# Optimization experiments

Measured on AMD Instinct MI355X. Metric: run time of the kernel, lower is better.

## Reference

```python
import jax, jax.numpy as jnp
import numpy as np
import math
from jax import lax

N, C, D = 16384, 1000, 512
CHUNK = 128  # tile size over samples for the L1 path (avoids NxCxD materialization)
EPS = 1e-8   # torch F.cosine_similarity eps


def setup_inputs() -> dict:
    key = jax.random.key(0)
    kf, kc = jax.random.split(key)
    features = jax.random.normal(kf, (N, D), dtype=jnp.float32)
    centroids = jax.random.normal(kc, (C, D), dtype=jnp.float32)
    return {"features": features, "centroids": centroids}


def _distances(features, centroids):
    n, d = features.shape
    scale = 1.0 / math.sqrt(d)

    # --- L1: cdist(p=1), computed in sample tiles to avoid an [N,C,D] tensor ---
    def l1_chunk(fc):  # fc: [CHUNK, D] -> [CHUNK, C]
        return jnp.sum(jnp.abs(fc[:, None, :] - centroids[None, :, :]), axis=-1)

    f_tiles = features.reshape(-1, CHUNK, d)
    l1 = lax.map(l1_chunk, f_tiles).reshape(n, -1) * scale

    # --- L2: cdist(p=2) via ||f||^2 + ||c||^2 - 2 f.c (GEMM fast path) ---
    f_sq = jnp.sum(features * features, axis=1)            # [N]
    c_sq = jnp.sum(centroids * centroids, axis=1)          # [C]
    dots = features @ centroids.T                          # [N, C]
    sq = jnp.maximum(f_sq[:, None] + c_sq[None, :] - 2.0 * dots, 0.0)
    l2 = jnp.sqrt(sq) * scale

    # --- cosine: F.cosine_similarity with per-vector norm clamped at EPS ---
    f_norm = jnp.maximum(jnp.sqrt(f_sq), EPS)              # [N]
    c_norm = jnp.maximum(jnp.sqrt(c_sq), EPS)              # [C]
    cos = (dots / (f_norm[:, None] * c_norm[None, :])) * scale

    return l1, l2, cos


def reference(features, centroids):
    return _distances(features, centroids)
```

## Files before the change

### kernel.cpp

```cpp
#include <hip/hip_runtime.h>
#include <math.h>

typedef float f32x4 __attribute__((ext_vector_type(4)));
typedef short s16x8 __attribute__((ext_vector_type(8)));

#define N_TOT 16384
#define C_TOT 1000
#define C_PAD 1024
#define D_TOT 512
#define NC ((size_t)N_TOT * C_TOT)

#define EPS_F 1e-8f
#define SCALE_F 0.04419417382415922f

#define GL_LDS(gp, lp)                                                        \
    __builtin_amdgcn_global_load_lds(                                         \
        (const __attribute__((address_space(1))) void*)(gp),                  \
        (__attribute__((address_space(3))) void*)(lp), 16, 0, 0)

__global__ __launch_bounds__(256)
void sq_kernel(const float* __restrict__ F, const float* __restrict__ Cc,
               float* __restrict__ sqout) {
    int gw   = (blockIdx.x * 256 + threadIdx.x) >> 6;
    int lane = threadIdx.x & 63;
    if (gw >= N_TOT + C_TOT) return;
    const float* src = (gw < N_TOT) ? (F + (size_t)gw * D_TOT)
                                    : (Cc + (size_t)(gw - N_TOT) * D_TOT);
    f32x4 a = *(const f32x4*)(src + lane * 4);
    f32x4 b = *(const f32x4*)(src + 256 + lane * 4);
    float acc = a[0] * a[0];
    acc = fmaf(a[1], a[1], acc);
    acc = fmaf(a[2], a[2], acc);
    acc = fmaf(a[3], a[3], acc);
    acc = fmaf(b[0], b[0], acc);
    acc = fmaf(b[1], b[1], acc);
    acc = fmaf(b[2], b[2], acc);
    acc = fmaf(b[3], b[3], acc);
    #pragma unroll
    for (int off = 32; off > 0; off >>= 1)
        acc += __shfl_xor(acc, off);
    if (lane == 0) sqout[gw] = acc;
}

__device__ inline short f2bf(float x) {
    union { float f; unsigned u; } v; v.f = x;
    unsigned r = (v.u + 0x7FFFu + ((v.u >> 16) & 1u)) >> 16;
    return (short)r;
}

__global__ __launch_bounds__(256)
void cvt_kernel(const float* __restrict__ F, const float* __restrict__ Cc,
                short* __restrict__ Fbf, short* __restrict__ Cbf) {
    const int FS8 = N_TOT * D_TOT / 8;
    const int CS8 = C_PAD * D_TOT / 8;
    int gid = blockIdx.x * 256 + threadIdx.x;
    if (gid < FS8) {
        const float* s = F + (size_t)gid * 8;
        f32x4 a = *(const f32x4*)s;
        f32x4 b = *(const f32x4*)(s + 4);
        s16x8 o;
        o[0] = f2bf(a[0]); o[1] = f2bf(a[1]); o[2] = f2bf(a[2]); o[3] = f2bf(a[3]);
        o[4] = f2bf(b[0]); o[5] = f2bf(b[1]); o[6] = f2bf(b[2]); o[7] = f2bf(b[3]);
        *(s16x8*)(Fbf + (size_t)gid * 8) = o;
    } else if (gid < FS8 + CS8) {
        int j = gid - FS8;
        int base = j * 8;
        int crow = base >> 9;
        s16x8 o = (s16x8)(short)0;
        if (crow < C_TOT) {
            const float* s = Cc + (size_t)base;
            f32x4 a = *(const f32x4*)s;
            f32x4 b = *(const f32x4*)(s + 4);
            o[0] = f2bf(a[0]); o[1] = f2bf(a[1]); o[2] = f2bf(a[2]); o[3] = f2bf(a[3]);
            o[4] = f2bf(b[0]); o[5] = f2bf(b[1]); o[6] = f2bf(b[2]); o[7] = f2bf(b[3]);
        }
        *(s16x8*)(Cbf + (size_t)base) = o;
    }
}

__global__ __launch_bounds__(256)
void dot_gemm(const short* __restrict__ Fbf, const short* __restrict__ Cbf,
              const float* __restrict__ sqbuf, float* __restrict__ out) {
    __shared__ short lds[2][8192];

    const int tid  = threadIdx.x;
    const int lane = tid & 63;
    const int wid  = tid >> 6;
    const int wr   = wid >> 1;
    const int wc   = wid & 1;
    const int m0   = blockIdx.y * 128;
    const int n0   = blockIdx.x * 128;

    const int row0 = tid >> 2;
    const int row1 = row0 + 64;
    const int slot = tid & 3;
    const int sw0  = slot ^ ((row0 >> 1) & 3);
    const int sw1  = slot ^ ((row1 >> 1) & 3);
    const short* sA0 = Fbf + (size_t)(m0 + row0) * D_TOT + sw0 * 8;
    const short* sA1 = Fbf + (size_t)(m0 + row1) * D_TOT + sw1 * 8;
    const short* sB0 = Cbf + (size_t)(n0 + row0) * D_TOT + sw0 * 8;
    const short* sB1 = Cbf + (size_t)(n0 + row1) * D_TOT + sw1 * 8;

    int offA[4], offB[4];
    #pragma unroll
    for (int fi = 0; fi < 4; ++fi) {
        int R = wr * 64 + fi * 16 + (lane & 15);
        offA[fi] = R * 32 + (((lane >> 4) ^ ((R >> 1) & 3)) << 3);
    }
    #pragma unroll
    for (int fj = 0; fj < 4; ++fj) {
        int R = wc * 64 + fj * 16 + (lane & 15);
        offB[fj] = 4096 + R * 32 + (((lane >> 4) ^ ((R >> 1) & 3)) << 3);
    }

    f32x4 acc[4][4];
    #pragma unroll
    for (int fi = 0; fi < 4; ++fi)
        #pragma unroll
        for (int fj = 0; fj < 4; ++fj) acc[fi][fj] = (f32x4)(0.f);

    GL_LDS(sA0, &lds[0][(size_t)tid * 8]);
    GL_LDS(sA1, &lds[0][(size_t)(tid + 256) * 8]);
    GL_LDS(sB0, &lds[0][4096 + (size_t)tid * 8]);
    GL_LDS(sB1, &lds[0][4096 + (size_t)(tid + 256) * 8]);
    __syncthreads();

    const int NK = D_TOT / 32;
    for (int kt = 0; kt < NK; ++kt) {
        if (kt + 1 < NK) {
            const int nb = (kt + 1) & 1;
            const int d1 = (kt + 1) * 32;
            GL_LDS(sA0 + d1, &lds[nb][(size_t)tid * 8]);
            GL_LDS(sA1 + d1, &lds[nb][(size_t)(tid + 256) * 8]);
            GL_LDS(sB0 + d1, &lds[nb][4096 + (size_t)tid * 8]);
            GL_LDS(sB1 + d1, &lds[nb][4096 + (size_t)(tid + 256) * 8]);
        }
        const short* lb = lds[kt & 1];
        s16x8 af[4], bg[4];
        #pragma unroll
        for (int fi = 0; fi < 4; ++fi) af[fi] = *(const s16x8*)&lb[offA[fi]];
        #pragma unroll
        for (int fj = 0; fj < 4; ++fj) bg[fj] = *(const s16x8*)&lb[offB[fj]];
        #pragma unroll
        for (int fi = 0; fi < 4; ++fi)
            #pragma unroll
            for (int fj = 0; fj < 4; ++fj)
                acc[fi][fj] = __builtin_amdgcn_mfma_f32_16x16x32_bf16(
                    af[fi], bg[fj], acc[fi][fj], 0, 0, 0);
        __syncthreads();
    }

    const float* csq = sqbuf + N_TOT;
    float fs_[4][4], fn_[4][4];
    #pragma unroll
    for (int fi = 0; fi < 4; ++fi)
        #pragma unroll
        for (int reg = 0; reg < 4; ++reg) {
            int m = m0 + wr * 64 + fi * 16 + ((lane >> 4) << 2) + reg;
            float v = sqbuf[m];
            fs_[fi][reg] = v;
            fn_[fi][reg] = fmaxf(sqrtf(v), EPS_F);
        }
    #pragma unroll
    for (int fj = 0; fj < 4; ++fj) {
        int c = n0 + wc * 64 + fj * 16 + (lane & 15);
        if (c < C_TOT) {
            float cs = csq[c];
            float cn = fmaxf(sqrtf(cs), EPS_F);
            #pragma unroll
            for (int fi = 0; fi < 4; ++fi) {
                int mrow = m0 + wr * 64 + fi * 16 + ((lane >> 4) << 2);
                #pragma unroll
                for (int reg = 0; reg < 4; ++reg) {
                    float d = acc[fi][fj][reg];
                    size_t p = (size_t)(mrow + reg) * C_TOT + c;
                    float sqv = fmaxf(fs_[fi][reg] + cs - 2.0f * d, 0.f);
                    out[NC + p]     = sqrtf(sqv) * SCALE_F;
                    out[2 * NC + p] = (d * SCALE_F) / (fn_[fi][reg] * cn);
                }
            }
        }
    }
}

__device__ inline void add_abs(float& acc, float d) {
    asm("v_add_f32 %0, %0, abs(%1)" : "+v"(acc) : "v"(d));
}

__global__ __launch_bounds__(256)
void l1_main(const float* __restrict__ F, const float* __restrict__ Cc,
             float* __restrict__ out) {
    __shared__ float lds[2][192 * 16];

    const int tid = threadIdx.x;
    const int tx  = tid & 15;
    const int ty  = tid >> 4;
    const int c0  = blockIdx.x * 64;
    const int n0  = blockIdx.y * 128;

    const int srow  = tid >> 2;
    const int sslot = tid & 3;
    const int w16   = (tid >> 6) * 16;

    const float* fA = F + (size_t)(n0 + srow) * D_TOT + sslot * 4;
    const float* fB = fA + (size_t)64 * D_TOT;
    const int cswz  = sslot ^ ((srow >> 2) & 3);
    const float* cP = Cc + (size_t)(c0 + srow) * D_TOT + cswz * 4;
    const bool cok  = (c0 + srow) < C_TOT;

    f32x4 l1v[8];
    #pragma unroll
    for (int i = 0; i < 8; ++i) l1v[i] = (f32x4)(0.f);

    GL_LDS(fA, &lds[0][w16 * 16]);
    GL_LDS(fB, &lds[0][(64 + w16) * 16]);
    if (cok) GL_LDS(cP, &lds[0][(128 + w16) * 16]);
    __syncthreads();

    const int NT  = 32;
    const int crs = (tx >> 2) & 3;

    for (int t = 0; t < NT; ++t) {
        if (t + 1 < NT) {
            const int nb = (t + 1) & 1;
            const int d1 = (t + 1) * 16;
            GL_LDS(fA + d1, &lds[nb][w16 * 16]);
            GL_LDS(fB + d1, &lds[nb][(64 + w16) * 16]);
            if (cok) GL_LDS(cP + d1, &lds[nb][(128 + w16) * 16]);
        }

        const float* lf = &lds[t & 1][0];
        #pragma unroll
        for (int q = 0; q < 4; ++q) {
            const int cq = (q ^ crs) << 2;
            f32x4 cv0 = *(const f32x4*)&lf[(128 + tx) * 16 + cq];
            f32x4 cv1 = *(const f32x4*)&lf[(128 + tx + 16) * 16 + cq];
            f32x4 cv2 = *(const f32x4*)&lf[(128 + tx + 32) * 16 + cq];
            f32x4 cv3 = *(const f32x4*)&lf[(128 + tx + 48) * 16 + cq];
            #pragma unroll
            for (int i = 0; i < 8; ++i) {
                f32x4 fv = *(const f32x4*)&lf[((ty + 16 * i) << 4) + (q << 2)];
                float a0 = l1v[i][0], a1 = l1v[i][1];
                float a2 = l1v[i][2], a3 = l1v[i][3];
                #pragma unroll
                for (int k = 0; k < 4; ++k) {
                    add_abs(a0, fv[k] - cv0[k]);
                    add_abs(a1, fv[k] - cv1[k]);
                    add_abs(a2, fv[k] - cv2[k]);
                    add_abs(a3, fv[k] - cv3[k]);
                }
                l1v[i][0] = a0; l1v[i][1] = a1;
                l1v[i][2] = a2; l1v[i][3] = a3;
            }
        }
        __syncthreads();
    }

    #pragma unroll
    for (int i = 0; i < 8; ++i) {
        const size_t rb = (size_t)(n0 + ty + 16 * i) * C_TOT;
        #pragma unroll
        for (int j = 0; j < 4; ++j) {
            const int c = c0 + tx + 16 * j;
            if (c < C_TOT) out[rb + c] = l1v[i][j] * SCALE_F;
        }
    }
}

extern "C" void kernel_launch(void* const* d_in, const int* in_sizes, int n_in,
                              void* d_out, int out_size, void* d_ws, size_t ws_size,
                              hipStream_t stream) {
    const float* F  = (const float*)d_in[0];
    const float* Cc = (const float*)d_in[1];
    float* out   = (float*)d_out;
    float* sqbuf = (float*)d_ws;

    short* Fbf = (short*)out;
    short* Cbf = Fbf + (size_t)N_TOT * D_TOT;

    int rows = N_TOT + C_TOT;
    sq_kernel<<<(rows + 3) / 4, 256, 0, stream>>>(F, Cc, sqbuf);
    cvt_kernel<<<(N_TOT * D_TOT / 8 + C_PAD * D_TOT / 8 + 255) / 256, 256, 0,
                 stream>>>(F, Cc, Fbf, Cbf);
    dot_gemm<<<dim3(8, 128), 256, 0, stream>>>(Fbf, Cbf, sqbuf, out);
    l1_main<<<dim3(16, 128), 256, 0, stream>>>(F, Cc, out);
}
```

Before: 377.0 us.

## Compute L1 distances in packed fp16 with a converted-input kernel

Adds a conversion kernel that writes fp16 copies of features and centroids into the workspace, and a new L1 kernel that uses packed v_pk_add_f16 subtract, abs via a mask, and accumulation, then reduces with fdot2 into fp32 per 32-element tile. The goal is to double L1 arithmetic throughput and halve LDS and global traffic compared with the fp32 L1 path. The path runs only when the workspace is large enough, otherwise it falls back to the old kernel. The cost is an extra conversion pass and fp16 rounding and accumulation error in the L1 results, which risks failing tolerance.

```diff
diff --git a/kernel.cpp b/kernel.cpp
--- a/kernel.cpp
+++ b/kernel.cpp
@@ -1,8 +1,10 @@
 #include <hip/hip_runtime.h>
 #include <math.h>
 
-typedef float f32x4 __attribute__((ext_vector_type(4)));
-typedef short s16x8 __attribute__((ext_vector_type(8)));
+typedef float    f32x4 __attribute__((ext_vector_type(4)));
+typedef unsigned u32x4 __attribute__((ext_vector_type(4)));
+typedef short    s16x8 __attribute__((ext_vector_type(8)));
+typedef _Float16 h2    __attribute__((ext_vector_type(2)));
 
 #define N_TOT 16384
 #define C_TOT 1000
@@ -79,6 +81,40 @@
 }
 
 __global__ __launch_bounds__(256)
+void cvt16_kernel(const float* __restrict__ F, const float* __restrict__ Cc,
+                  short* __restrict__ Ff16, short* __restrict__ Cf16) {
+    const int FS8 = N_TOT * D_TOT / 8;
+    const int CS8 = C_PAD * D_TOT / 8;
+    int gid = blockIdx.x * 256 + threadIdx.x;
+    if (gid < FS8) {
+        const float* s = F + (size_t)gid * 8;
+        f32x4 a = *(const f32x4*)s;
+        f32x4 b = *(const f32x4*)(s + 4);
+        u32x4 w;
+        w[0] = __builtin_bit_cast(unsigned, __builtin_amdgcn_cvt_pkrtz(a[0], a[1]));
+        w[1] = __builtin_bit_cast(unsigned, __builtin_amdgcn_cvt_pkrtz(a[2], a[3]));
+        w[2] = __builtin_bit_cast(unsigned, __builtin_amdgcn_cvt_pkrtz(b[0], b[1]));
+        w[3] = __builtin_bit_cast(unsigned, __builtin_amdgcn_cvt_pkrtz(b[2], b[3]));
+        *(u32x4*)(Ff16 + (size_t)gid * 8) = w;
+    } else if (gid < FS8 + CS8) {
+        int j = gid - FS8;
+        int base = j * 8;
+        int crow = base >> 9;
+        u32x4 w = (u32x4)(0u);
+        if (crow < C_TOT) {
+            const float* s = Cc + (size_t)base;
+            f32x4 a = *(const f32x4*)s;
+            f32x4 b = *(const f32x4*)(s + 4);
+            w[0] = __builtin_bit_cast(unsigned, __builtin_amdgcn_cvt_pkrtz(a[0], a[1]));
+            w[1] = __builtin_bit_cast(unsigned, __builtin_amdgcn_cvt_pkrtz(a[2], a[3]));
+            w[2] = __builtin_bit_cast(unsigned, __builtin_amdgcn_cvt_pkrtz(b[0], b[1]));
+            w[3] = __builtin_bit_cast(unsigned, __builtin_amdgcn_cvt_pkrtz(b[2], b[3]));
+        }
+        *(u32x4*)(Cf16 + (size_t)base) = w;
+    }
+}
+
+__global__ __launch_bounds__(256)
 void dot_gemm(const short* __restrict__ Fbf, const short* __restrict__ Cbf,
               const float* __restrict__ sqbuf, float* __restrict__ out) {
     __shared__ short lds[2][8192];
@@ -267,21 +303,118 @@
     }
 }
 
+__global__ __launch_bounds__(256)
+void l1_f16(const short* __restrict__ Ff16, const short* __restrict__ Cf16,
+            float* __restrict__ out) {
+    __shared__ char lds[2][192 * 64];
+
+    const int tid = threadIdx.x;
+    const int tx  = tid & 15;
+    const int ty  = tid >> 4;
+    const int c0  = blockIdx.x * 64;
+    const int n0  = blockIdx.y * 128;
+
+    const int r0 = tid >> 2;
+    const int s0 = tid & 3;
+    const int w16 = (tid >> 6) * 16;
+
+    const short* gF0 = Ff16 + (size_t)(n0 + r0) * D_TOT + s0 * 8;
+    const short* gF1 = gF0 + (size_t)64 * D_TOT;
+    const int cswz   = s0 ^ ((r0 >> 2) & 3);
+    const short* gC  = Cf16 + (size_t)(c0 + r0) * D_TOT + cswz * 8;
+
+    f32x4 l1v[8];
+    #pragma unroll
+    for (int i = 0; i < 8; ++i) l1v[i] = (f32x4)(0.f);
+
+    GL_LDS(gF0, &lds[0][w16 * 64]);
+    GL_LDS(gF1, &lds[0][(64 + w16) * 64]);
+    GL_LDS(gC,  &lds[0][(128 + w16) * 64]);
+    __syncthreads();
+
+    const int NT  = 16;
+    const int crs = (tx >> 2) & 3;
+    const h2 ones = {(_Float16)1.0f, (_Float16)1.0f};
+
+    for (int t = 0; t < NT; ++t) {
+        if (t + 1 < NT) {
+            const int nb = (t + 1) & 1;
+            const int d1 = (t + 1) * 32;
+            GL_LDS(gF0 + d1, &lds[nb][w16 * 64]);
+            GL_LDS(gF1 + d1, &lds[nb][(64 + w16) * 64]);
+            GL_LDS(gC + d1,  &lds[nb][(128 + w16) * 64]);
+        }
+
+        const char* lf = lds[t & 1];
+        #pragma unroll
+        for (int j = 0; j < 4; ++j) {
+            unsigned accp[8];
+            #pragma unroll
+            for (int i = 0; i < 8; ++i) accp[i] = 0u;
+            #pragma unroll
+            for (int q = 0; q < 4; ++q) {
+                u32x4 cw = *(const u32x4*)(lf + (128 + tx + 16 * j) * 64 +
+                                           ((q ^ crs) << 4));
+                #pragma unroll
+                for (int i = 0; i < 8; ++i) {
+                    u32x4 fw = *(const u32x4*)(lf + (ty + 16 * i) * 64 + (q << 4));
+                    #pragma unroll
+                    for (int m = 0; m < 4; ++m) {
+                        unsigned d;
+                        asm("v_pk_add_f16 %0, %1, %2 neg_lo:[0,1] neg_hi:[0,1]"
+                            : "=v"(d) : "v"(fw[m]), "v"(cw[m]));
+                        d &= 0x7FFF7FFFu;
+                        asm("v_pk_add_f16 %0, %0, %1"
+                            : "+v"(accp[i]) : "v"(d));
+                    }
+                }
+            }
+            #pragma unroll
+            for (int i = 0; i < 8; ++i)
+                l1v[i][j] = __builtin_amdgcn_fdot2(
+                    __builtin_bit_cast(h2, accp[i]), ones, l1v[i][j], false);
+        }
+        __syncthreads();
+    }
+
+    #pragma unroll
+    for (int i = 0; i < 8; ++i) {
+        const size_t rb = (size_t)(n0 + ty + 16 * i) * C_TOT;
+        #pragma unroll
+        for (int j = 0; j < 4; ++j) {
+            const int c = c0 + tx + 16 * j;
+            if (c < C_TOT) out[rb + c] = l1v[i][j] * SCALE_F;
+        }
+    }
+}
+
 extern "C" void kernel_launch(void* const* d_in, const int* in_sizes, int n_in,
                               void* d_out, int out_size, void* d_ws, size_t ws_size,
                               hipStream_t stream) {
     const float* F  = (const float*)d_in[0];
     const float* Cc = (const float*)d_in[1];
     float* out   = (float*)d_out;
-    float* sqbuf = (float*)d_ws;
+    char*  wsb   = (char*)d_ws;
+    float* sqbuf = (float*)wsb;
 
     short* Fbf = (short*)out;
     short* Cbf = Fbf + (size_t)N_TOT * D_TOT;
 
+    const size_t F16_OFF = 131072;
+    short* Ff16 = (short*)(wsb + F16_OFF);
+    short* Cf16 = Ff16 + (size_t)N_TOT * D_TOT;
+    const size_t ws_need = F16_OFF + (size_t)(N_TOT + C_PAD) * D_TOT * 2;
+    const bool fast = ws_size >= ws_need;
+
     int rows = N_TOT + C_TOT;
+    int cvt_grid = (N_TOT * D_TOT / 8 + C_PAD * D_TOT / 8 + 255) / 256;
     sq_kernel<<<(rows + 3) / 4, 256, 0, stream>>>(F, Cc, sqbuf);
-    cvt_kernel<<<(N_TOT * D_TOT / 8 + C_PAD * D_TOT / 8 + 255) / 256, 256, 0,
-                 stream>>>(F, Cc, Fbf, Cbf);
+    cvt_kernel<<<cvt_grid, 256, 0, stream>>>(F, Cc, Fbf, Cbf);
+    if (fast)
+        cvt16_kernel<<<cvt_grid, 256, 0, stream>>>(F, Cc, Ff16, Cf16);
     dot_gemm<<<dim3(8, 128), 256, 0, stream>>>(Fbf, Cbf, sqbuf, out);
-    l1_main<<<dim3(16, 128), 256, 0, stream>>>(F, Cc, out);
-}
+    if (fast)
+        l1_f16<<<dim3(16, 128), 256, 0, stream>>>(Ff16, Cf16, out);
+    else
+        l1_main<<<dim3(16, 128), 256, 0, stream>>>(F, Cc, out);
+}
```

After: 464.7 us. 23.3% more time.
